# Performance work log

Measured on AMD Instinct MI355X. Metric: run time of the kernel, lower is better.

The kernel has to match this reference:

```python
import jax, jax.numpy as jnp
import numpy as np

N = 100000        # nodes
E_INTRA = 800000  # intra (covalent) edges
E_INTER = 400000  # inter (protein-ligand) edges
NODE_DIM = 35
H = 128           # hidden_dim
G = 256           # graphs in batch
N_LAYERS = 4
BN_EPS = 1e-5

seg_sum = jax.ops.segment_sum


def setup_inputs() -> dict:
    key = jax.random.key(0)
    ks = jax.random.split(key, 24)
    s = 1.0 / np.sqrt(H)
    inp = {
        "x": jax.random.normal(ks[0], (N, NODE_DIM), jnp.float32),
        "edge_index_intra": jax.random.randint(ks[1], (2, E_INTRA), 0, N, jnp.int32),
        "edge_index_inter": jax.random.randint(ks[2], (2, E_INTER), 0, N, jnp.int32),
        "pos": jax.random.normal(ks[3], (N, 3), jnp.float32),
        "edge_attr": jax.random.uniform(ks[4], (E_INTRA, 1), jnp.float32),
        "batch": jnp.sort(jax.random.randint(ks[5], (N,), 0, G, jnp.int32)),
        # lin_node
        "lin_node_W": jax.random.normal(ks[6], (NODE_DIM, H), jnp.float32) / np.sqrt(NODE_DIM),
        "lin_node_b": jnp.zeros((H,), jnp.float32),
        # 4 DVNHIL layers (stacked)
        "W_intra": jax.random.normal(ks[7], (N_LAYERS, H, H), jnp.float32) * s,
        "b_intra": jnp.zeros((N_LAYERS, H), jnp.float32),
        "W_inter": jax.random.normal(ks[8], (N_LAYERS, H, H), jnp.float32) * s,
        "b_inter": jnp.zeros((N_LAYERS, H), jnp.float32),
        # FC head: 3 hidden linears + BN affine, then output linear to 1 task
        "fc_W": jax.random.normal(ks[9], (3, H, H), jnp.float32) * s,
        "fc_b": jnp.zeros((3, H), jnp.float32),
        "bn_gamma": jnp.ones((3, H), jnp.float32),
        "bn_beta": jnp.zeros((3, H), jnp.float32),
        "out_W": jax.random.normal(ks[10], (H, 1), jnp.float32) * s,
        "out_b": jnp.zeros((1,), jnp.float32),
    }
    return inp


def reference(x, edge_index_intra, edge_index_inter, pos, edge_attr, batch,
              lin_node_W, lin_node_b, W_intra, b_intra, W_inter, b_inter,
              fc_W, fc_b, bn_gamma, bn_beta, out_W, out_b):
    src_i, dst_i = edge_index_intra[0], edge_index_intra[1]
    src_e, dst_e = edge_index_inter[0], edge_index_inter[1]

    # lin_node: Linear + SiLU
    h = jax.nn.silu(x @ lin_node_W + lin_node_b)  # [N, H]

    # degrees of destination nodes (scatter-add of ones)
    ones_i = jnp.ones((src_i.shape[0],), h.dtype)
    ones_e = jnp.ones((src_e.shape[0],), h.dtype)
    deg_intra = seg_sum(ones_i, dst_i, num_segments=N)[:, None]           # [N,1]
    deg_inter = jnp.log(seg_sum(ones_e, dst_e, num_segments=N)[:, None] + 1.0)

    # geometric weight on inter edges from pos
    d2 = jnp.sum((pos[src_e] - pos[dst_e]) ** 2, axis=-1, keepdims=True)  # [E_inter,1]
    w_inter = jnp.exp(-d2)

    v_p = jnp.zeros_like(h)
    v_l = jnp.zeros_like(h)
    for i in range(N_LAYERS):
        # intra: gather -> edge-weighted transform -> scatter-add -> degree norm
        m_i = (h[src_i] * edge_attr) @ W_intra[i] + b_intra[i]            # [E_intra,H]
        m_i = seg_sum(m_i, dst_i, num_segments=N) / (deg_intra + 1.0)
        # inter: gather -> distance-weighted transform -> scatter-add -> log-degree scale
        m_e = (h[src_e] * w_inter) @ W_inter[i] + b_inter[i]              # [E_inter,H]
        m_e = seg_sum(m_e, dst_e, num_segments=N) * deg_inter
        v_p = jax.nn.silu(m_i + v_p)
        v_l = jax.nn.silu(m_e + v_l)
        h = h + v_p + v_l

    # global_add_pool over graphs
    g = seg_sum(h, batch, num_segments=G)  # [G, H]

    # FC head (eval mode: dropout identity, BN with running mean=0/var=1)
    bn_scale = 1.0 / jnp.sqrt(1.0 + BN_EPS)
    for j in range(3):
        g = jax.nn.leaky_relu(g @ fc_W[j] + fc_b[j], negative_slope=0.01)
        g = g * bn_scale * bn_gamma[j] + bn_beta[j]
    out = g @ out_W + out_b  # [G, 1]
    return out.reshape(-1)
```

## Files before the change

### kernel.cpp

```cpp
#include <hip/hip_runtime.h>
#include <math.h>

#define NN 100000
#define EIN 800000
#define EEX 400000
#define ND 35
#define H 128
#define NG 256
#define NL 4
#define TM 16
#define TML 16
#define NTILES 6250
#define CAPI 32
#define CAPE 16
#define OVFCAP 16384

typedef unsigned short u16;
typedef unsigned char u8;
typedef short s8v __attribute__((ext_vector_type(8)));
typedef float f4v __attribute__((ext_vector_type(4)));
typedef float f2v __attribute__((ext_vector_type(2)));

__device__ __forceinline__ float silu_f(float x){ return x / (1.0f + __expf(-x)); }
__device__ __forceinline__ float bf2f(u16 v){ return __uint_as_float(((unsigned)v) << 16); }
__device__ __forceinline__ float bfw_lo(unsigned u){ return __uint_as_float(u << 16); }
__device__ __forceinline__ float bfw_hi(unsigned u){ return __uint_as_float(u & 0xffff0000u); }
__device__ __forceinline__ u16 f2bf(float f){
  unsigned u = __float_as_uint(f);
  u += 0x7FFFu + ((u >> 16) & 1u);
  return (u16)(u >> 16);
}
__device__ __forceinline__ u8 f2fp8(float f){
  int p = __builtin_amdgcn_cvt_pk_fp8_f32(f, f, 0, false);
  return (u8)(p & 0xff);
}
__device__ __forceinline__ unsigned pk_bf16(float lo, float hi){
  unsigned r;
  asm("v_cvt_pk_bf16_f32 %0, %1, %2" : "=v"(r) : "v"(lo), "v"(hi));
  return r;
}

__global__ __launch_bounds__(256) void k_prep(const float* __restrict__ x,
                                              const float* __restrict__ lnW,
                                              const float* __restrict__ lnb,
                                              u16* __restrict__ h,
                                              u8* __restrict__ h8,
                                              const float* __restrict__ WI,
                                              const float* __restrict__ WE,
                                              u16* __restrict__ WfI,
                                              u16* __restrict__ WfE,
                                              const int* __restrict__ src_i,
                                              const int* __restrict__ dst_i,
                                              const float* __restrict__ ea,
                                              const int* __restrict__ src_e,
                                              const int* __restrict__ dst_e,
                                              const float* __restrict__ pos,
                                              int* __restrict__ cnt_i,
                                              int* __restrict__ cnt_e,
                                              int2* __restrict__ bktI,
                                              int2* __restrict__ bktE,
                                              int* __restrict__ ovfhdr,
                                              int4* __restrict__ ovfList){
  const int NBW = 2*NL;
  const int NBL = NN/TML;
  if (blockIdx.x < NBW){
    const int lm = blockIdx.x;
    const int l = lm >> 1;
    const float* src = (lm & 1) ? (WE + (size_t)l*H*H) : (WI + (size_t)l*H*H);
    u16* dst = ((lm & 1) ? WfE : WfI) + (size_t)l*H*H;
    for (int idx = threadIdx.x; idx < H*H; idx += 256){
      const int r = idx & 7, lane = (idx>>3)&63, kc = (idx>>9)&3, jt = idx>>11;
      const int k = kc*32 + (lane>>4)*8 + r;
      const int j = jt*16 + (lane&15);
      dst[idx] = f2bf(src[k*H + j]);
    }
    return;
  }
  if (blockIdx.x < NBW + NBL){
    __shared__ u16 xs[TM][72];
    const int n0 = (blockIdx.x - NBW) * TML;
    const int tid = threadIdx.x;
    for (int i = tid; i < TM*64; i += 256){
      const int m = i >> 6, k = i & 63;
      xs[m][k] = (k < ND) ? f2bf(x[(size_t)(n0+m)*ND + k]) : (u16)0;
    }
    __syncthreads();
    const int lane = tid & 63;
    const int wv   = tid >> 6;
    const int col  = lane & 15;
    const int quad = lane >> 4;
    const int jta = 2*wv, jtb = 2*wv + 1;
    const int ja = jta*16 + col, jb = jtb*16 + col;

    f4v accA = {0.f,0.f,0.f,0.f}, accB = {0.f,0.f,0.f,0.f};
    #pragma unroll
    for (int kc = 0; kc < 2; ++kc){
      const s8v a = *(const s8v*)&xs[col][kc*32 + quad*8];
      s8v bA, bB;
      #pragma unroll
      for (int r = 0; r < 8; ++r){
        const int k = kc*32 + quad*8 + r;
        bA[r] = (k < ND) ? (short)f2bf(lnW[k*H + ja]) : (short)0;
        bB[r] = (k < ND) ? (short)f2bf(lnW[k*H + jb]) : (short)0;
      }
      accA = __builtin_amdgcn_mfma_f32_16x16x32_bf16(a, bA, accA, 0, 0, 0);
      accB = __builtin_amdgcn_mfma_f32_16x16x32_bf16(a, bB, accB, 0, 0, 0);
    }
    const float bja = lnb[ja], bjb = lnb[jb];
    #pragma unroll
    for (int r = 0; r < 4; ++r){
      const int n = n0 + quad*4 + r;
      const float ha = silu_f(accA[r] + bja);
      const float hb = silu_f(accB[r] + bjb);
      h[(size_t)n*H + ja] = f2bf(ha);
      h[(size_t)n*H + jb] = f2bf(hb);
      h8[(size_t)n*H + ja] = f2fp8(ha);
      h8[(size_t)n*H + jb] = f2fp8(hb);
    }
    return;
  }
  int e = (blockIdx.x - NBW - NBL)*256 + threadIdx.x;
  if (e < EIN){
    const int s = src_i[e], d = dst_i[e];
    const int wbits = __float_as_int(ea[e]);
    const int slot = atomicAdd(&cnt_i[d], 1);
    if (slot < CAPI) bktI[((size_t)d << 5) + slot] = make_int2(s, wbits);
    else {
      const int oi = atomicAdd(ovfhdr, 1);
      if (oi < OVFCAP) ovfList[oi] = make_int4(d, s, wbits, 0);
    }
  } else if (e < EIN + EEX){
    const int ee = e - EIN;
    const int s = src_e[ee], d = dst_e[ee];
    const float dx = pos[3*s+0] - pos[3*d+0];
    const float dy = pos[3*s+1] - pos[3*d+1];
    const float dz = pos[3*s+2] - pos[3*d+2];
    const float w = __expf(-(dx*dx + dy*dy + dz*dz));
    const int wbits = __float_as_int(w);
    const int slot = atomicAdd(&cnt_e[d], 1);
    if (slot < CAPE) bktE[((size_t)d << 4) + slot] = make_int2(s, wbits);
    else {
      const int oi = atomicAdd(ovfhdr, 1);
      if (oi < OVFCAP) ovfList[oi] = make_int4(d, s, wbits, 1);
    }
  }
}

#define ACCONE(qx, qy, vv, A0, A1, A2, A3) {                                          \
    const f2v x01 = __builtin_amdgcn_cvt_pk_f32_fp8((int)(qx), false);                \
    const f2v x23 = __builtin_amdgcn_cvt_pk_f32_fp8((int)(qx), true);                 \
    const f2v x45 = __builtin_amdgcn_cvt_pk_f32_fp8((int)(qy), false);                \
    const f2v x67 = __builtin_amdgcn_cvt_pk_f32_fp8((int)(qy), true);                 \
    A0 += x01 * (vv); A1 += x23 * (vv); A2 += x45 * (vv); A3 += x67 * (vv); }

#define GATHER_SHARED_DECL                                                            \
  __shared__ __align__(16) char smem_[16896];                                         \
  u16 (*aggIs)[136] = (u16(*)[136])(smem_);                                           \
  u16 (*aggEs)[136] = (u16(*)[136])(smem_ + 4352);                                    \
  int2 (*edI)[CAPI] = (int2(*)[CAPI])(smem_ + 8704);              \
  int2 (*edE)[CAPE] = (int2(*)[CAPE])(smem_ + 12800);             \
  float (*mif)[132] = (float(*)[132])(smem_);                                         \
  float (*mef)[132] = (float(*)[132])(smem_ + 8448);

#define GATHER_DECLS                                                                  \
  const int slot = tid >> 4;                                                          \
  const int l16  = tid & 15;                                                          \
  const int j8 = l16 * 8;                                                             \
  const int n = n0 + slot;                                                            \
  const int cIv = cntI[n];                                                            \
  const int cEv = cntE[n];

#define GATHER_LDS_BODY                                                               \
  {                                                                                   \
    const int uI = cIv < CAPI ? cIv : CAPI;                                           \
    const int uE = cEv < CAPE ? cEv : CAPE;                                           \
    const int pIv = (uI + 7) & ~7;                                                    \
    const int pEv = (uE + 3) & ~3;                                                    \
    {                                                                                 \
      const size_t bI_ = ((size_t)n << 5);                                            \
      for (int t = l16; t < pIv; t += 16)                                             \
        edI[slot][t] = (t < uI) ? bktI[bI_ + t] : make_int2(0, 0);                    \
      const size_t bE_ = ((size_t)n << 4);                                            \
      for (int t = l16; t < pEv; t += 16)                                             \
        edE[slot][t] = (t < uE) ? bktE[bE_ + t] : make_int2(0, 0);                    \
    }                                                                                 \
    __syncthreads();                                                                  \
    f2v aI0={0.f,0.f}, aI1={0.f,0.f}, aI2={0.f,0.f}, aI3={0.f,0.f};                   \
    f2v aE0={0.f,0.f}, aE1={0.f,0.f}, aE2={0.f,0.f}, aE3={0.f,0.f};                   \
    {                                                                                 \
      const int nbI_ = pIv >> 3, nbE_ = pEv >> 2;                                     \
      const int nb = nbI_ > nbE_ ? nbI_ : nbE_;                                       \
      int tIi = 0, tEi = 0;                                                           \
      for (int b = 0; b < nb; ++b){                                                   \
        const bool doI = b < nbI_;                                                    \
        const bool doE = b < nbE_;                                                    \
        int2 eIr[8]; uint2 qIr[8]; int2 eEr[4]; uint2 qEr[4];                         \
        if (doI){                                                                     \
          _Pragma("unroll")                                                           \
          for (int k = 0; k < 8; ++k) eIr[k] = edI[slot][tIi + k];                    \
          _Pragma("unroll")                                                           \
          for (int k = 0; k < 8; ++k){                                                \
            const unsigned off = ((unsigned)eIr[k].x << 7) | (unsigned)j8;            \
            qIr[k] = *(const uint2*)(hin8 + off);                                     \
          }                                                                           \
        }                                                                             \
        if (doE){                                                                     \
          _Pragma("unroll")                                                           \
          for (int k = 0; k < 4; ++k) eEr[k] = edE[slot][tEi + k];                    \
          _Pragma("unroll")                                                           \
          for (int k = 0; k < 4; ++k){                                                \
            const unsigned off = ((unsigned)eEr[k].x << 7) | (unsigned)j8;            \
            qEr[k] = *(const uint2*)(hin8 + off);                                     \
          }                                                                           \
        }                                                                             \
        if (doI){                                                                     \
          _Pragma("unroll")                                                           \
          for (int k = 0; k < 8; ++k){                                                \
            const float v = __int_as_float(eIr[k].y);                                 \
            ACCONE(qIr[k].x, qIr[k].y, v, aI0, aI1, aI2, aI3)                         \
          }                                                                           \
          tIi += 8;                                                                   \
        }                                                                             \
        if (doE){                                                                     \
          _Pragma("unroll")                                                           \
          for (int k = 0; k < 4; ++k){                                                \
            const float v = __int_as_float(eEr[k].y);                                 \
            ACCONE(qEr[k].x, qEr[k].y, v, aE0, aE1, aE2, aE3)                         \
          }                                                                           \
          tEi += 4;                                                                   \
        }                                                                             \
      }                                                                               \
    }                                                                                 \
    const int nov = ovfhdr[0];                                                        \
    if (__builtin_expect(nov > 0, 0)){                                                \
      const int novc = nov < OVFCAP ? nov : OVFCAP;                                   \
      for (int o = 0; o < novc; ++o){                                                 \
        const int4 E = ovfList[o];                                                    \
        if (E.x == n){                                                                \
          const unsigned off = ((unsigned)E.y << 7) | (unsigned)j8;                   \
          const uint2 q = *(const uint2*)(hin8 + off);                                \
          const float v = __int_as_float(E.z);                                        \
          if (E.w == 0){ ACCONE(q.x, q.y, v, aI0, aI1, aI2, aI3) }                    \
          else         { ACCONE(q.x, q.y, v, aE0, aE1, aE2, aE3) }                    \
        }                                                                             \
      }                                                                               \
    }                                                                                 \
    *(uint4*)&aggIs[slot][j8] = make_uint4(pk_bf16(aI0.x, aI0.y), pk_bf16(aI1.x, aI1.y), \
                                           pk_bf16(aI2.x, aI2.y), pk_bf16(aI3.x, aI3.y)); \
    *(uint4*)&aggEs[slot][j8] = make_uint4(pk_bf16(aE0.x, aE0.y), pk_bf16(aE1.x, aE1.y), \
                                           pk_bf16(aE2.x, aE2.y), pk_bf16(aE3.x, aE3.y)); \
  }

#define MFMA_BODY                                                                     \
  f4v accIA = {0.f,0.f,0.f,0.f}, accIB = {0.f,0.f,0.f,0.f};                           \
  f4v accEA = {0.f,0.f,0.f,0.f}, accEB = {0.f,0.f,0.f,0.f};                           \
  _Pragma("unroll")                                                                   \
  for (int kc = 0; kc < 4; ++kc){                                                     \
    const int koff = kc*32 + quad*8;                                                  \
    const s8v aI = *(const s8v*)&aggIs[col][koff];                                    \
    const s8v aE = *(const s8v*)&aggEs[col][koff];                                    \
    const s8v bIA = *(const s8v*)(WfI + (((jta*4 + kc)*64 + lane) << 3));             \
    const s8v bIB = *(const s8v*)(WfI + (((jtb*4 + kc)*64 + lane) << 3));             \
    const s8v bEA = *(const s8v*)(WfE + (((jta*4 + kc)*64 + lane) << 3));             \
    const s8v bEB = *(const s8v*)(WfE + (((jtb*4 + kc)*64 + lane) << 3));             \
    accIA = __builtin_amdgcn_mfma_f32_16x16x32_bf16(aI, bIA, accIA, 0, 0, 0);         \
    accIB = __builtin_amdgcn_mfma_f32_16x16x32_bf16(aI, bIB, accIB, 0, 0, 0);         \
    accEA = __builtin_amdgcn_mfma_f32_16x16x32_bf16(aE, bEA, accEA, 0, 0, 0);         \
    accEB = __builtin_amdgcn_mfma_f32_16x16x32_bf16(aE, bEB, accEB, 0, 0, 0);         \
  }

#define ACC2LDS                                                                       \
  __syncthreads();                                                                    \
  _Pragma("unroll")                                                                   \
  for (int r = 0; r < 4; ++r){                                                        \
    mif[quad*4+r][jta*16+col] = accIA[r];                                             \
    mif[quad*4+r][jtb*16+col] = accIB[r];                                             \
    mef[quad*4+r][jta*16+col] = accEA[r];                                             \
    mef[quad*4+r][jtb*16+col] = accEB[r];                                             \
  }                                                                                   \
  __syncthreads();

#define EPI_COMMON                                                                    \
  const float cIf = (float)cIv;                                                       \
  const float cEf = (float)cEv;                                                       \
  const float rdI = 1.0f / (cIf + 1.0f);                                              \
  const float ldE = __logf(cEf + 1.0f);                                               \
  const f4v miA = *(const f4v*)&mif[slot][j8];                                        \
  const f4v miB = *(const f4v*)&mif[slot][j8+4];                                      \
  const f4v meA = *(const f4v*)&mef[slot][j8];                                        \
  const f4v meB = *(const f4v*)&mef[slot][j8+4];                                      \
  const f4v bIa_ = *(const f4v*)(bI + j8);                                            \
  const f4v bIb_ = *(const f4v*)(bI + j8 + 4);                                        \
  const f4v bEa_ = *(const f4v*)(bE + j8);                                            \
  const f4v bEb_ = *(const f4v*)(bE + j8 + 4);                                        \
  const unsigned idx8 = (unsigned)n*H + (unsigned)j8;

#define STORE_STATE8                                                                  \
  uint4 vps, vls, hs;                                                                 \
  vps.x = pk_bf16(vpn[0],vpn[1]); vps.y = pk_bf16(vpn[2],vpn[3]);                     \
  vps.z = pk_bf16(vpn[4],vpn[5]); vps.w = pk_bf16(vpn[6],vpn[7]);                     \
  vls.x = pk_bf16(vln[0],vln[1]); vls.y = pk_bf16(vln[2],vln[3]);                     \
  vls.z = pk_bf16(vln[4],vln[5]); vls.w = pk_bf16(vln[6],vln[7]);                     \
  hs.x = pk_bf16(hnew[0],hnew[1]); hs.y = pk_bf16(hnew[2],hnew[3]);                   \
  hs.z = pk_bf16(hnew[4],hnew[5]); hs.w = pk_bf16(hnew[6],hnew[7]);                   \
  *(uint4*)(vp + idx8) = vps;                                                         \
  *(uint4*)(vl + idx8) = vls;                                                         \
  *(uint4*)(hout + idx8) = hs;                                                        \
  int d0_ = __builtin_amdgcn_cvt_pk_fp8_f32(hnew[0], hnew[1], 0, false);              \
  d0_ = __builtin_amdgcn_cvt_pk_fp8_f32(hnew[2], hnew[3], d0_, true);                 \
  int d1_ = __builtin_amdgcn_cvt_pk_fp8_f32(hnew[4], hnew[5], 0, false);              \
  d1_ = __builtin_amdgcn_cvt_pk_fp8_f32(hnew[6], hnew[7], d1_, true);                 \
  uint2 h8s; h8s.x = (unsigned)d0_; h8s.y = (unsigned)d1_;                            \
  *(uint2*)(hout8 + idx8) = h8s;

__global__ __launch_bounds__(256, 4) void k_layer(
    const u16* __restrict__ hin, const u8* __restrict__ hin8,
    u16* __restrict__ hout, u8* __restrict__ hout8,
    u16* __restrict__ vp, u16* __restrict__ vl,
    const int* __restrict__ cntI, const int* __restrict__ cntE,
    const int2* __restrict__ bktI, const int2* __restrict__ bktE,
    const int* __restrict__ ovfhdr, const int4* __restrict__ ovfList,
    const u16* __restrict__ WfI, const float* __restrict__ bI,
    const u16* __restrict__ WfE, const float* __restrict__ bE)
{
  GATHER_SHARED_DECL
  const int n0 = blockIdx.x * TM;
  const int tid = threadIdx.x;
  GATHER_DECLS
  GATHER_LDS_BODY
  __syncthreads();

  const int lane = tid & 63;
  const int w    = tid >> 6;
  const int jta = 2*w, jtb = 2*w + 1;
  const int col  = lane & 15;
  const int quad = lane >> 4;
  MFMA_BODY
  ACC2LDS

  EPI_COMMON
  const uint4 vpq = *(const uint4*)(vp + idx8);
  const uint4 vlq = *(const uint4*)(vl + idx8);
  const uint4 hq  = *(const uint4*)(hin + idx8);
  const unsigned vpw[4] = {vpq.x, vpq.y, vpq.z, vpq.w};
  const unsigned vlw[4] = {vlq.x, vlq.y, vlq.z, vlq.w};
  const unsigned hwv[4] = {hq.x, hq.y, hq.z, hq.w};
  float vpn[8], vln[8], hnew[8];
  #pragma unroll
  for (int k = 0; k < 8; ++k){
    const float miv = (k < 4) ? miA[k] : miB[k-4];
    const float mev = (k < 4) ? meA[k] : meB[k-4];
    const float bIv = (k < 4) ? bIa_[k] : bIb_[k-4];
    const float bEv = (k < 4) ? bEa_[k] : bEb_[k-4];
    const float mi = (miv + cIf*bIv) * rdI;
    const float me = (mev + cEf*bEv) * ldE;
    const float vpo = (k & 1) ? bfw_hi(vpw[k>>1]) : bfw_lo(vpw[k>>1]);
    const float vlo = (k & 1) ? bfw_hi(vlw[k>>1]) : bfw_lo(vlw[k>>1]);
    const float ho  = (k & 1) ? bfw_hi(hwv[k>>1]) : bfw_lo(hwv[k>>1]);
    vpn[k] = silu_f(mi + vpo);
    vln[k] = silu_f(me + vlo);
    hnew[k] = ho + vpn[k] + vln[k];
  }
  STORE_STATE8
}

__global__ __launch_bounds__(256, 4) void k_layer0(
    const u16* __restrict__ hin, const u8* __restrict__ hin8,
    u16* __restrict__ hout, u8* __restrict__ hout8,
    u16* __restrict__ vp, u16* __restrict__ vl,
    const int* __restrict__ cntI, const int* __restrict__ cntE,
    const int2* __restrict__ bktI, const int2* __restrict__ bktE,
    const int* __restrict__ ovfhdr, const int4* __restrict__ ovfList,
    const u16* __restrict__ WfI, const float* __restrict__ bI,
    const u16* __restrict__ WfE, const float* __restrict__ bE)
{
  GATHER_SHARED_DECL
  const int n0 = blockIdx.x * TM;
  const int tid = threadIdx.x;
  GATHER_DECLS
  GATHER_LDS_BODY
  __syncthreads();

  const int lane = tid & 63;
  const int w    = tid >> 6;
  const int jta = 2*w, jtb = 2*w + 1;
  const int col  = lane & 15;
  const int quad = lane >> 4;
  MFMA_BODY
  ACC2LDS

  EPI_COMMON
  const uint4 hq = *(const uint4*)(hin + idx8);
  const unsigned hwv[4] = {hq.x, hq.y, hq.z, hq.w};
  float vpn[8], vln[8], hnew[8];
  #pragma unroll
  for (int k = 0; k < 8; ++k){
    const float miv = (k < 4) ? miA[k] : miB[k-4];
    const float mev = (k < 4) ? meA[k] : meB[k-4];
    const float bIv = (k < 4) ? bIa_[k] : bIb_[k-4];
    const float bEv = (k < 4) ? bEa_[k] : bEb_[k-4];
    const float mi = (miv + cIf*bIv) * rdI;
    const float me = (mev + cEf*bEv) * ldE;
    const float ho = (k & 1) ? bfw_hi(hwv[k>>1]) : bfw_lo(hwv[k>>1]);
    vpn[k] = silu_f(mi);
    vln[k] = silu_f(me);
    hnew[k] = ho + vpn[k] + vln[k];
  }
  STORE_STATE8
}

__global__ __launch_bounds__(256, 4) void k_layer3(
    const u16* __restrict__ hin, const u8* __restrict__ hin8,
    u16* __restrict__ vp, u16* __restrict__ vl,
    const int* __restrict__ cntI, const int* __restrict__ cntE,
    const int2* __restrict__ bktI, const int2* __restrict__ bktE,
    const int* __restrict__ ovfhdr, const int4* __restrict__ ovfList,
    const u16* __restrict__ WfI, const float* __restrict__ bI,
    const u16* __restrict__ WfE, const float* __restrict__ bE,
    const int* __restrict__ batch, float* __restrict__ gp)
{
  GATHER_SHARED_DECL
  const int n0 = blockIdx.x * TM;
  const int tid = threadIdx.x;
  GATHER_DECLS
  GATHER_LDS_BODY
  __syncthreads();

  const int lane = tid & 63;
  const int w    = tid >> 6;
  const int jta = 2*w, jtb = 2*w + 1;
  const int col  = lane & 15;
  const int quad = lane >> 4;
  MFMA_BODY
  ACC2LDS

  EPI_COMMON
  const uint4 vpq = *(const uint4*)(vp + idx8);
  const uint4 vlq = *(const uint4*)(vl + idx8);
  const uint4 hq  = *(const uint4*)(hin + idx8);
  const unsigned vpw[4] = {vpq.x, vpq.y, vpq.z, vpq.w};
  const unsigned vlw[4] = {vlq.x, vlq.y, vlq.z, vlq.w};
  const unsigned hwv[4] = {hq.x, hq.y, hq.z, hq.w};
  float hnew[8];
  #pragma unroll
  for (int k = 0; k < 8; ++k){
    const float miv = (k < 4) ? miA[k] : miB[k-4];
    const float mev = (k < 4) ? meA[k] : meB[k-4];
    const float bIv = (k < 4) ? bIa_[k] : bIb_[k-4];
    const float bEv = (k < 4) ? bEa_[k] : bEb_[k-4];
    const float mi = (miv + cIf*bIv) * rdI;
    const float me = (mev + cEf*bEv) * ldE;
    const float vpo = (k & 1) ? bfw_hi(vpw[k>>1]) : bfw_lo(vpw[k>>1]);
    const float vlo = (k & 1) ? bfw_hi(vlw[k>>1]) : bfw_lo(vlw[k>>1]);
    const float ho  = (k & 1) ? bfw_hi(hwv[k>>1]) : bfw_lo(hwv[k>>1]);
    const float vpn = silu_f(mi + vpo);
    const float vln = silu_f(me + vlo);
    hnew[k] = ho + vpn + vln;
  }

  const int b0 = batch[n0];
  const int b15 = batch[n0 + TM - 1];
  if (b0 == b15){
    #pragma unroll
    for (int k = 0; k < 8; ++k){
      hnew[k] += __shfl_xor(hnew[k], 16, 64);
      hnew[k] += __shfl_xor(hnew[k], 32, 64);
    }
    __syncthreads();
    if (quad == 0){
      f4v s0 = {hnew[0], hnew[1], hnew[2], hnew[3]};
      f4v s1 = {hnew[4], hnew[5], hnew[6], hnew[7]};
      *(f4v*)&mif[w][j8] = s0;
      *(f4v*)&mif[w][j8+4] = s1;
    }
    __syncthreads();
    if (tid < 128){
      const float s = mif[0][tid] + mif[1][tid] + mif[2][tid] + mif[3][tid];
      atomicAdd(&gp[(size_t)b0*H + tid], s);
    }
  } else {
    const int bn = batch[n];
    #pragma unroll
    for (int k = 0; k < 8; ++k)
      atomicAdd(&gp[(size_t)bn*H + j8 + k], hnew[k]);
  }
}

__global__ void k_fc(const float* __restrict__ g, const float* __restrict__ fcW,
                     const float* __restrict__ fcb, const float* __restrict__ gamma,
                     const float* __restrict__ beta, const float* __restrict__ outW,
                     const float* __restrict__ outb, float* __restrict__ out){
  __shared__ float row[H];
  __shared__ float red[H];
  const int gi = blockIdx.x;
  const int j = threadIdx.x;
  row[j] = g[(size_t)gi*H + j];
  __syncthreads();
  const float bn_scale = rsqrtf(1.0f + 1e-5f);
  for (int l = 0; l < 3; ++l){
    const float* W = fcW + (size_t)l*H*H;
    float acc = fcb[l*H + j];
    #pragma unroll 8
    for (int k = 0; k < H; ++k) acc += row[k] * W[k*H + j];
    acc = (acc > 0.f) ? acc : 0.01f*acc;
    acc = acc * bn_scale * gamma[l*H + j] + beta[l*H + j];
    __syncthreads();
    row[j] = acc;
    __syncthreads();
  }
  red[j] = row[j] * outW[j];
  __syncthreads();
  for (int o = 64; o > 0; o >>= 1){
    if (j < o) red[j] += red[j + o];
    __syncthreads();
  }
  if (j == 0) out[gi] = red[0] + outb[0];
}

extern "C" void kernel_launch(void* const* d_in, const int* in_sizes, int n_in,
                              void* d_out, int out_size, void* d_ws, size_t ws_size,
                              hipStream_t stream)
{
  const float* x    = (const float*)d_in[0];
  const int*   eii  = (const int*)  d_in[1];
  const int*   eie  = (const int*)  d_in[2];
  const float* pos  = (const float*)d_in[3];
  const float* ea   = (const float*)d_in[4];
  const int*   batch= (const int*)  d_in[5];
  const float* lnW  = (const float*)d_in[6];
  const float* lnb  = (const float*)d_in[7];
  const float* WIa  = (const float*)d_in[8];
  const float* bIa  = (const float*)d_in[9];
  const float* WEa  = (const float*)d_in[10];
  const float* bEa  = (const float*)d_in[11];
  const float* fcW  = (const float*)d_in[12];
  const float* fcb  = (const float*)d_in[13];
  const float* gam  = (const float*)d_in[14];
  const float* bet  = (const float*)d_in[15];
  const float* outW = (const float*)d_in[16];
  const float* outb = (const float*)d_in[17];
  float* out = (float*)d_out;

  const int* src_i = eii;  const int* dst_i = eii + EIN;
  const int* src_e = eie;  const int* dst_e = eie + EEX;

  const size_t NH = (size_t)NN * H;
  u16* hA = (u16*)d_ws;
  u16* hB = hA + NH;
  u16* vp = hB + NH;
  u16* vl = vp + NH;
  u8* hA8 = (u8*)(vl + NH);
  u8* hB8 = hA8 + NH;
  float* gp = (float*)(hB8 + NH);
  int* cnt_i = (int*)(gp + (size_t)NG*H);
  int* cnt_e = cnt_i + NN;
  int* ovfhdr = cnt_e + NN;
  int4* ovfList = (int4*)(ovfhdr + 4);
  int2* bktI = (int2*)(ovfList + OVFCAP);
  int2* bktE = bktI + (size_t)NN*CAPI;
  u16* WfI = (u16*)(bktE + (size_t)NN*CAPE);
  u16* WfE = WfI + (size_t)NL*H*H;

  const size_t need = (size_t)((char*)(WfE + (size_t)NL*H*H) - (char*)d_ws);
  if (ws_size < need) return;

  hipMemsetAsync(gp, 0, ((size_t)NG*H + 2*(size_t)NN + 4)*sizeof(int), stream);

  const int NE_ALL = EIN + EEX;
  const int NBF = (NE_ALL + 255)/256;
  k_prep<<<2*NL + NN/TML + NBF, 256, 0, stream>>>(x, lnW, lnb, hA, hA8, WIa, WEa, WfI, WfE,
                                                  src_i, dst_i, ea, src_e, dst_e, pos,
                                                  cnt_i, cnt_e, bktI, bktE, ovfhdr, ovfList);

  k_layer0<<<NTILES, 256, 0, stream>>>(hA, hA8, hB, hB8, vp, vl,
      cnt_i, cnt_e, bktI, bktE, ovfhdr, ovfList,
      WfI + 0*(size_t)H*H, bIa + 0*H, WfE + 0*(size_t)H*H, bEa + 0*H);
  k_layer<<<NTILES, 256, 0, stream>>>(hB, hB8, hA, hA8, vp, vl,
      cnt_i, cnt_e, bktI, bktE, ovfhdr, ovfList,
      WfI + 1*(size_t)H*H, bIa + 1*H, WfE + 1*(size_t)H*H, bEa + 1*H);
  k_layer<<<NTILES, 256, 0, stream>>>(hA, hA8, hB, hB8, vp, vl,
      cnt_i, cnt_e, bktI, bktE, ovfhdr, ovfList,
      WfI + 2*(size_t)H*H, bIa + 2*H, WfE + 2*(size_t)H*H, bEa + 2*H);
  k_layer3<<<NTILES, 256, 0, stream>>>(hB, hB8, vp, vl,
      cnt_i, cnt_e, bktI, bktE, ovfhdr, ovfList,
      WfI + 3*(size_t)H*H, bIa + 3*H, WfE + 3*(size_t)H*H, bEa + 3*H,
      batch, gp);

  k_fc<<<NG, H, 0, stream>>>(gp, fcW, fcb, gam, bet, outW, outb, out);
}
```

Measured before the change: 444.5 us.

## Pack edge bucket entries into 32-bit words and widen gather batches

```diff
diff --git a/kernel.cpp b/kernel.cpp
--- a/kernel.cpp
+++ b/kernel.cpp
@@ -14,6 +14,7 @@
 #define CAPI 32
 #define CAPE 16
 #define OVFCAP 16384
+#define EPT 8
 
 typedef unsigned short u16;
 typedef unsigned char u8;
@@ -38,6 +39,9 @@
   unsigned r;
   asm("v_cvt_pk_bf16_f32 %0, %1, %2" : "=v"(r) : "v"(lo), "v"(hi));
   return r;
+}
+__device__ __forceinline__ unsigned pack_ew(int s, float w){
+  return ((unsigned)s << 15) | (unsigned)f2bf(w);
 }
 
 __global__ __launch_bounds__(256) void k_prep(const float* __restrict__ x,
@@ -57,8 +61,8 @@
                                               const float* __restrict__ pos,
                                               int* __restrict__ cnt_i,
                                               int* __restrict__ cnt_e,
-                                              int2* __restrict__ bktI,
-                                              int2* __restrict__ bktE,
+                                              unsigned* __restrict__ bktI,
+                                              unsigned* __restrict__ bktE,
                                               int* __restrict__ ovfhdr,
                                               int4* __restrict__ ovfList){
   const int NBW = 2*NL;
@@ -119,29 +123,50 @@
     }
     return;
   }
-  int e = (blockIdx.x - NBW - NBL)*256 + threadIdx.x;
-  if (e < EIN){
-    const int s = src_i[e], d = dst_i[e];
-    const int wbits = __float_as_int(ea[e]);
-    const int slot = atomicAdd(&cnt_i[d], 1);
-    if (slot < CAPI) bktI[((size_t)d << 5) + slot] = make_int2(s, wbits);
-    else {
-      const int oi = atomicAdd(ovfhdr, 1);
-      if (oi < OVFCAP) ovfList[oi] = make_int4(d, s, wbits, 0);
-    }
-  } else if (e < EIN + EEX){
-    const int ee = e - EIN;
-    const int s = src_e[ee], d = dst_e[ee];
-    const float dx = pos[3*s+0] - pos[3*d+0];
-    const float dy = pos[3*s+1] - pos[3*d+1];
-    const float dz = pos[3*s+2] - pos[3*d+2];
-    const float w = __expf(-(dx*dx + dy*dy + dz*dz));
-    const int wbits = __float_as_int(w);
-    const int slot = atomicAdd(&cnt_e[d], 1);
-    if (slot < CAPE) bktE[((size_t)d << 4) + slot] = make_int2(s, wbits);
-    else {
-      const int oi = atomicAdd(ovfhdr, 1);
-      if (oi < OVFCAP) ovfList[oi] = make_int4(d, s, wbits, 1);
+  const int NE_ALL_ = EIN + EEX;
+  const int base = (blockIdx.x - NBW - NBL)*(256*EPT) + (int)threadIdx.x;
+  int eV[EPT], sV[EPT], dV[EPT];
+  #pragma unroll
+  for (int k = 0; k < EPT; ++k){
+    const int e = base + k*256;
+    eV[k] = e;
+    int s = 0, d = 0;
+    if (e < EIN){ s = src_i[e]; d = dst_i[e]; }
+    else if (e < NE_ALL_){ s = src_e[e-EIN]; d = dst_e[e-EIN]; }
+    sV[k] = s; dV[k] = d;
+  }
+  float wV[EPT];
+  #pragma unroll
+  for (int k = 0; k < EPT; ++k){
+    const int e = eV[k];
+    float w = 0.f;
+    if (e < EIN) w = ea[e];
+    else if (e < NE_ALL_){
+      const int s = sV[k], d = dV[k];
+      const float dx = pos[3*s+0] - pos[3*d+0];
+      const float dy = pos[3*s+1] - pos[3*d+1];
+      const float dz = pos[3*s+2] - pos[3*d+2];
+      w = __expf(-(dx*dx + dy*dy + dz*dz));
+    }
+    wV[k] = w;
+  }
+  #pragma unroll
+  for (int k = 0; k < EPT; ++k){
+    const int e = eV[k];
+    if (e < EIN){
+      const int slot = atomicAdd(&cnt_i[dV[k]], 1);
+      if (slot < CAPI) bktI[((size_t)dV[k] << 5) + slot] = pack_ew(sV[k], wV[k]);
+      else {
+        const int oi = atomicAdd(ovfhdr, 1);
+        if (oi < OVFCAP) ovfList[oi] = make_int4(dV[k], sV[k], __float_as_int(wV[k]), 0);
+      }
+    } else if (e < NE_ALL_){
+      const int slot = atomicAdd(&cnt_e[dV[k]], 1);
+      if (slot < CAPE) bktE[((size_t)dV[k] << 4) + slot] = pack_ew(sV[k], wV[k]);
+      else {
+        const int oi = atomicAdd(ovfhdr, 1);
+        if (oi < OVFCAP) ovfList[oi] = make_int4(dV[k], sV[k], __float_as_int(wV[k]), 1);
+      }
     }
   }
 }
@@ -157,8 +182,8 @@
   __shared__ __align__(16) char smem_[16896];                                         \
   u16 (*aggIs)[136] = (u16(*)[136])(smem_);                                           \
   u16 (*aggEs)[136] = (u16(*)[136])(smem_ + 4352);                                    \
-  int2 (*edI)[CAPI] = (int2(*)[CAPI])(smem_ + 8704);              \
-  int2 (*edE)[CAPE] = (int2(*)[CAPE])(smem_ + 12800);             \
+  unsigned (*edI)[CAPI] = (unsigned(*)[CAPI])(smem_ + 8704);      \
+  unsigned (*edE)[CAPE] = (unsigned(*)[CAPE])(smem_ + 10752);     \
   float (*mif)[132] = (float(*)[132])(smem_);                                         \
   float (*mef)[132] = (float(*)[132])(smem_ + 8448);
 
@@ -174,60 +199,62 @@
   {                                                                                   \
     const int uI = cIv < CAPI ? cIv : CAPI;                                           \
     const int uE = cEv < CAPE ? cEv : CAPE;                                           \
-    const int pIv = (uI + 7) & ~7;                                                    \
-    const int pEv = (uE + 3) & ~3;                                                    \
+    const int pIv = (uI + 15) & ~15;                                                  \
+    const int pEv = (uE + 7) & ~7;                                                    \
     {                                                                                 \
       const size_t bI_ = ((size_t)n << 5);                                            \
       for (int t = l16; t < pIv; t += 16)                                             \
-        edI[slot][t] = (t < uI) ? bktI[bI_ + t] : make_int2(0, 0);                    \
+        edI[slot][t] = (t < uI) ? bktI[bI_ + t] : 0u;                                 \
       const size_t bE_ = ((size_t)n << 4);                                            \
-      for (int t = l16; t < pEv; t += 16)                                             \
-        edE[slot][t] = (t < uE) ? bktE[bE_ + t] : make_int2(0, 0);                    \
+      if (l16 < pEv)                                                                  \
+        edE[slot][l16] = (l16 < uE) ? bktE[bE_ + l16] : 0u;                           \
     }                                                                                 \
     __syncthreads();                                                                  \
     f2v aI0={0.f,0.f}, aI1={0.f,0.f}, aI2={0.f,0.f}, aI3={0.f,0.f};                   \
     f2v aE0={0.f,0.f}, aE1={0.f,0.f}, aE2={0.f,0.f}, aE3={0.f,0.f};                   \
     {                                                                                 \
-      const int nbI_ = pIv >> 3, nbE_ = pEv >> 2;                                     \
+      const int nbI_ = pIv >> 4, nbE_ = pEv >> 3;                                     \
       const int nb = nbI_ > nbE_ ? nbI_ : nbE_;                                       \
       int tIi = 0, tEi = 0;                                                           \
       for (int b = 0; b < nb; ++b){                                                   \
         const bool doI = b < nbI_;                                                    \
         const bool doE = b < nbE_;                                                    \
-        int2 eIr[8]; uint2 qIr[8]; int2 eEr[4]; uint2 qEr[4];                         \
+        unsigned eIw[16], eEw[8]; uint2 qI[16], qE[8];                                \
         if (doI){                                                                     \
+          *(uint4*)&eIw[0]  = *(const uint4*)&edI[slot][tIi+0];                       \
+          *(uint4*)&eIw[4]  = *(const uint4*)&edI[slot][tIi+4];                       \
+          *(uint4*)&eIw[8]  = *(const uint4*)&edI[slot][tIi+8];                       \
+          *(uint4*)&eIw[12] = *(const uint4*)&edI[slot][tIi+12];                      \
           _Pragma("unroll")                                                           \
-          for (int k = 0; k < 8; ++k) eIr[k] = edI[slot][tIi + k];                    \
-          _Pragma("unroll")                                                           \
-          for (int k = 0; k < 8; ++k){                                                \
-            const unsigned off = ((unsigned)eIr[k].x << 7) | (unsigned)j8;            \
-            qIr[k] = *(const uint2*)(hin8 + off);                                     \
+          for (int k = 0; k < 16; ++k){                                               \
+            const unsigned off = ((eIw[k] >> 15) << 7) | (unsigned)j8;                \
+            qI[k] = *(const uint2*)(hin8 + off);                                      \
           }                                                                           \
         }                                                                             \
         if (doE){                                                                     \
+          *(uint4*)&eEw[0] = *(const uint4*)&edE[slot][tEi+0];                        \
+          *(uint4*)&eEw[4] = *(const uint4*)&edE[slot][tEi+4];                        \
           _Pragma("unroll")                                                           \
-          for (int k = 0; k < 4; ++k) eEr[k] = edE[slot][tEi + k];                    \
-          _Pragma("unroll")                                                           \
-          for (int k = 0; k < 4; ++k){                                                \
-            const unsigned off = ((unsigned)eEr[k].x << 7) | (unsigned)j8;            \
-            qEr[k] = *(const uint2*)(hin8 + off);                                     \
+          for (int k = 0; k < 8; ++k){                                                \
+            const unsigned off = ((eEw[k] >> 15) << 7) | (unsigned)j8;                \
+            qE[k] = *(const uint2*)(hin8 + off);                                      \
           }                                                                           \
         }                                                                             \
         if (doI){                                                                     \
           _Pragma("unroll")                                                           \
-          for (int k = 0; k < 8; ++k){                                                \
-            const float v = __int_as_float(eIr[k].y);                                 \
-            ACCONE(qIr[k].x, qIr[k].y, v, aI0, aI1, aI2, aI3)                         \
+          for (int k = 0; k < 16; ++k){                                               \
+            const float v = __uint_as_float((eIw[k] & 0x7fffu) << 16);                \
+            ACCONE(qI[k].x, qI[k].y, v, aI0, aI1, aI2, aI3)                           \
           }                                                                           \
-          tIi += 8;                                                                   \
+          tIi += 16;                                                                  \
         }                                                                             \
         if (doE){                                                                     \
           _Pragma("unroll")                                                           \
-          for (int k = 0; k < 4; ++k){                                                \
-            const float v = __int_as_float(eEr[k].y);                                 \
-            ACCONE(qEr[k].x, qEr[k].y, v, aE0, aE1, aE2, aE3)                         \
+          for (int k = 0; k < 8; ++k){                                                \
+            const float v = __uint_as_float((eEw[k] & 0x7fffu) << 16);                \
+            ACCONE(qE[k].x, qE[k].y, v, aE0, aE1, aE2, aE3)                           \
           }                                                                           \
-          tEi += 4;                                                                   \
+          tEi += 8;                                                                   \
         }                                                                             \
       }                                                                               \
     }                                                                                 \
@@ -313,12 +340,12 @@
   uint2 h8s; h8s.x = (unsigned)d0_; h8s.y = (unsigned)d1_;                            \
   *(uint2*)(hout8 + idx8) = h8s;
 
-__global__ __launch_bounds__(256, 4) void k_layer(
+__global__ __launch_bounds__(256, 3) void k_layer(
     const u16* __restrict__ hin, const u8* __restrict__ hin8,
     u16* __restrict__ hout, u8* __restrict__ hout8,
     u16* __restrict__ vp, u16* __restrict__ vl,
     const int* __restrict__ cntI, const int* __restrict__ cntE,
-    const int2* __restrict__ bktI, const int2* __restrict__ bktE,
+    const unsigned* __restrict__ bktI, const unsigned* __restrict__ bktE,
     const int* __restrict__ ovfhdr, const int4* __restrict__ ovfList,
     const u16* __restrict__ WfI, const float* __restrict__ bI,
     const u16* __restrict__ WfE, const float* __restrict__ bE)
@@ -364,12 +391,12 @@
   STORE_STATE8
 }
 
-__global__ __launch_bounds__(256, 4) void k_layer0(
+__global__ __launch_bounds__(256, 3) void k_layer0(
     const u16* __restrict__ hin, const u8* __restrict__ hin8,
     u16* __restrict__ hout, u8* __restrict__ hout8,
     u16* __restrict__ vp, u16* __restrict__ vl,
     const int* __restrict__ cntI, const int* __restrict__ cntE,
-    const int2* __restrict__ bktI, const int2* __restrict__ bktE,
+    const unsigned* __restrict__ bktI, const unsigned* __restrict__ bktE,
     const int* __restrict__ ovfhdr, const int4* __restrict__ ovfList,
     const u16* __restrict__ WfI, const float* __restrict__ bI,
     const u16* __restrict__ WfE, const float* __restrict__ bE)
@@ -409,11 +436,11 @@
   STORE_STATE8
 }
 
-__global__ __launch_bounds__(256, 4) void k_layer3(
+__global__ __launch_bounds__(256, 3) void k_layer3(
     const u16* __restrict__ hin, const u8* __restrict__ hin8,
     u16* __restrict__ vp, u16* __restrict__ vl,
     const int* __restrict__ cntI, const int* __restrict__ cntE,
-    const int2* __restrict__ bktI, const int2* __restrict__ bktE,
+    const unsigned* __restrict__ bktI, const unsigned* __restrict__ bktE,
     const int* __restrict__ ovfhdr, const int4* __restrict__ ovfList,
     const u16* __restrict__ WfI, const float* __restrict__ bI,
     const u16* __restrict__ WfE, const float* __restrict__ bE,
@@ -556,8 +583,8 @@
   int* cnt_e = cnt_i + NN;
   int* ovfhdr = cnt_e + NN;
   int4* ovfList = (int4*)(ovfhdr + 4);
-  int2* bktI = (int2*)(ovfList + OVFCAP);
-  int2* bktE = bktI + (size_t)NN*CAPI;
+  unsigned* bktI = (unsigned*)(ovfList + OVFCAP);
+  unsigned* bktE = bktI + (size_t)NN*CAPI;
   u16* WfI = (u16*)(bktE + (size_t)NN*CAPE);
   u16* WfE = WfI + (size_t)NL*H*H;
 
@@ -567,7 +594,7 @@
   hipMemsetAsync(gp, 0, ((size_t)NG*H + 2*(size_t)NN + 4)*sizeof(int), stream);
 
   const int NE_ALL = EIN + EEX;
-  const int NBF = (NE_ALL + 255)/256;
+  const int NBF = (NE_ALL + 256*EPT - 1)/(256*EPT);
   k_prep<<<2*NL + NN/TML + NBF, 256, 0, stream>>>(x, lnW, lnb, hA, hA8, WIa, WEa, WfI, WfE,
                                                   src_i, dst_i, ea, src_e, dst_e, pos,
                                                   cnt_i, cnt_e, bktI, bktE, ovfhdr, ovfList);
```

Result: slower. 464.1 us (+4.4%).
